# Optimization experiments

Hardware: AMD Instinct MI355X
Metric: run time of the kernel (lower is better)

## Reference

```python
import jax, jax.numpy as jnp
import numpy as np

NUM_HEADS = 8
HEAD_DIM = 96
SCALE = HEAD_DIM ** -0.5
STRIDE_Q = (1, 2, 2)
STRIDE_KV = (1, 8, 8)
PAD = [(1, 1), (1, 1), (1, 1)]  # kernel 3 -> padding = 3//2 = 1


def _gelu_pool(t, w, stride, thw):
    """_pre_attention_pool -> GELU -> depthwise Conv3d -> _post_attention_pool.

    t: [B, H, L, hd] flattened tokens; thw = (T, Hs, Ws) with L = T*Hs*Ws.
    Returns pooled [B, H, L', hd] and new thw.
    """
    B, NH, L, C = t.shape
    T, Hs, Ws = thw
    x = t.reshape(B * NH, T, Hs, Ws, C).transpose(0, 4, 1, 2, 3)  # [B*NH, C, T, Hs, Ws]
    x = jax.nn.gelu(x, approximate=False)  # torch F.gelu default (erf)
    x = jax.lax.conv_general_dilated(
        x, w, window_strides=stride, padding=PAD,
        dimension_numbers=('NCDHW', 'OIDHW', 'NCDHW'),
        feature_group_count=C)  # depthwise: groups = head_dim
    new_thw = (x.shape[2], x.shape[3], x.shape[4])
    Lp = new_thw[0] * new_thw[1] * new_thw[2]
    x = x.reshape(B, NH, C, Lp).transpose(0, 1, 3, 2)  # [B, NH, L', C]
    return x, new_thw


def setup_inputs() -> dict:
    key = jax.random.key(0)
    ks = jax.random.split(key, 8)
    B, T, Hs, Ws, C = 2, 8, 56, 56, 768
    L = T * Hs * Ws
    s = 0.02
    return {
        'x': jax.random.normal(ks[0], (B, L, C), jnp.float32),
        'qkv_w': jax.random.normal(ks[1], (3 * C, C), jnp.float32) * s,
        'qkv_b': jnp.zeros((3 * C,), jnp.float32),
        'proj_w': jax.random.normal(ks[2], (C, C), jnp.float32) * s,
        'proj_b': jnp.zeros((C,), jnp.float32),
        'pool_q_w': jax.random.normal(ks[3], (HEAD_DIM, 1, 3, 3, 3), jnp.float32) * 0.1,
        'pool_k_w': jax.random.normal(ks[4], (HEAD_DIM, 1, 3, 3, 3), jnp.float32) * 0.1,
        'pool_v_w': jax.random.normal(ks[5], (HEAD_DIM, 1, 3, 3, 3), jnp.float32) * 0.1,
        't_size': T, 'h_size': Hs, 'w_size': Ws,
    }


def reference(x, qkv_w, qkv_b, proj_w, proj_b, pool_q_w, pool_k_w, pool_v_w,
              t_size, h_size, w_size):
    B, N, C = x.shape
    # fused qkv projection -> [3, B, heads, N, head_dim]
    qkv = (x @ qkv_w.T + qkv_b).reshape(B, N, 3, NUM_HEADS, C // NUM_HEADS)
    qkv = qkv.transpose(2, 0, 3, 1, 4)
    q, k, v = qkv[0], qkv[1], qkv[2]

    thw = (t_size, h_size, w_size)
    q, q_thw = _gelu_pool(q, pool_q_w, STRIDE_Q, thw)
    k, _ = _gelu_pool(k, pool_k_w, STRIDE_KV, thw)
    v, _ = _gelu_pool(v, pool_v_w, STRIDE_KV, thw)

    attn = jax.nn.softmax((q * SCALE) @ jnp.swapaxes(k, -2, -1), axis=-1)
    Nq = q.shape[2]
    out = (attn @ v + q)  # residual_pool=True (iMViT)
    out = out.transpose(0, 2, 1, 3).reshape(B, Nq, C)
    out = out @ proj_w.T + proj_b
    return out
```

## Files before the change

### kernel.cpp

```cpp
#include <hip/hip_runtime.h>
#include <cstdint>

#define NH 8
#define HD 96
#define CDIM 768
#define BQ 2
#define T0 8
#define H0 56
#define W0 56
#define L0 (T0*H0*W0)
#define HP_Q 28
#define WP_Q 28
#define LQ (T0*HP_Q*WP_Q)
#define HP_K 7
#define WP_K 7
#define LK (T0*HP_K*WP_K)
#define LKP 416
#define SCALE 0.10206207261596577f
#define NYC 20
#define MKV 6400

typedef __bf16 bf16;
typedef bf16 bf16x4 __attribute__((ext_vector_type(4)));
typedef bf16 bf16x8 __attribute__((ext_vector_type(8)));
typedef float f32x4 __attribute__((ext_vector_type(4)));
typedef float f4 __attribute__((ext_vector_type(4)));

#define GPTR(x) ((const __attribute__((address_space(1))) void*)(x))
#define LPTR(x) ((__attribute__((address_space(3))) void*)(x))

__device__ __forceinline__ float fast_gelu(float x) {
    float z = __builtin_fabsf(x) * 0.7071067811865476f;
    float p = 1.f + z*(0.278393f + z*(0.230389f + z*(0.000972f + z*0.078108f)));
    p = p * p;
    p = p * p;
    float e = 1.f - __builtin_amdgcn_rcpf(p);
    float erfv = (x < 0.f) ? -e : e;
    return 0.5f * x * (1.f + erfv);
}

#define NX4 9633792
#define NW4 442368
#define NP4 147456
__global__ void cvt_all(const f4* __restrict__ x, const f4* __restrict__ wq,
                        const f4* __restrict__ wp, bf16x4* __restrict__ xo,
                        bf16x4* __restrict__ wqo, bf16x4* __restrict__ wpo) {
    const long total = (long)NX4 + NW4 + NP4;
    long stride = (long)gridDim.x * blockDim.x;
    for (long i = (long)blockIdx.x * blockDim.x + threadIdx.x; i < total; i += stride) {
        f4 v; bf16x4* o;
        if (i < NX4)            { v = x[i];            o = xo + i; }
        else if (i < NX4 + NW4) { v = wq[i - NX4];     o = wqo + (i - NX4); }
        else                    { v = wp[i - NX4 - NW4]; o = wpo + (i - NX4 - NW4); }
        bf16x4 t;
        t.x = (bf16)v.x; t.y = (bf16)v.y; t.z = (bf16)v.z; t.w = (bf16)v.w;
        *o = t;
    }
}

__device__ __forceinline__ int cmap(int i) {
    return ((i + 1) / 3) * 8 + (i + 1) % 3 - 1;
}

__global__ __launch_bounds__(512, 2) void gemm256_q(
    const bf16* __restrict__ A, const bf16* __restrict__ B,
    const float* __restrict__ bias, bf16* __restrict__ Out)
{
    __shared__ bf16 sh[2*32768];
    const int tid = threadIdx.x;
    const int lane = tid & 63;
    const int wid = tid >> 6;
    const int wm = wid >> 2, wn = wid & 3;
    const int arow = lane & 15;
    const int g = lane >> 4;
    const int srow = tid >> 3;
    const int schunk = tid & 7;
    const int csw = schunk ^ (srow & 7);
    const int K = 768;

    const int nwg = gridDim.x;
    const int q_ = nwg >> 3, r_ = nwg & 7;
    const int xcd = blockIdx.x & 7, off = blockIdx.x >> 3;
    const int swz = (xcd < r_ ? xcd*(q_+1) : r_*(q_+1) + (xcd - r_)*q_) + off;
    const long bn = swz % 3, bm = swz / 3;

    f32x4 acc[8][4];
#pragma unroll
    for (int i = 0; i < 8; ++i)
#pragma unroll
        for (int j = 0; j < 4; ++j) acc[i][j] = (f32x4){0.f,0.f,0.f,0.f};

    const bf16* Ab = A + (bm*256 + srow)*(long)K + csw*8;
    const bf16* Bb = B + (bn*256 + srow)*(long)K + csw*8;

    auto issueA = [&](int buf, int kt, int s) {
        __builtin_amdgcn_global_load_lds(GPTR(Ab + (long)(s*64)*K + kt*64),
            LPTR(sh + buf*32768 + s*4096 + tid*8), 16, 0, 0);
    };
    auto issueB = [&](int buf, int kt, int s) {
        __builtin_amdgcn_global_load_lds(GPTR(Bb + (long)(s*64)*K + kt*64),
            LPTR(sh + buf*32768 + 16384 + s*4096 + tid*8), 16, 0, 0);
    };
    auto phase = [&](int buf, int qm, int qn) {
        const bf16* ldsA = sh + buf*32768;
        const bf16* ldsB = sh + buf*32768 + 16384;
        bf16x8 af[4][2], bfr[2][2];
#pragma unroll
        for (int i = 0; i < 4; ++i) {
            int R = wm*128 + (qm*4 + i)*16 + arow;
#pragma unroll
            for (int kk = 0; kk < 2; ++kk)
                af[i][kk] = *(const bf16x8*)&ldsA[R*64 + (((kk*4 + g) ^ (R & 7))*8)];
        }
#pragma unroll
        for (int j = 0; j < 2; ++j) {
            int R = wn*64 + (qn*2 + j)*16 + arow;
#pragma unroll
            for (int kk = 0; kk < 2; ++kk)
                bfr[j][kk] = *(const bf16x8*)&ldsB[R*64 + (((kk*4 + g) ^ (R & 7))*8)];
        }
        asm volatile("s_waitcnt lgkmcnt(0)" ::: "memory");
        __builtin_amdgcn_sched_barrier(0);
        __builtin_amdgcn_s_setprio(1);
#pragma unroll
        for (int i = 0; i < 4; ++i)
#pragma unroll
            for (int j = 0; j < 2; ++j)
#pragma unroll
                for (int kk = 0; kk < 2; ++kk)
                    acc[qm*4 + i][qn*2 + j] = __builtin_amdgcn_mfma_f32_16x16x32_bf16(
                        af[i][kk], bfr[j][kk], acc[qm*4 + i][qn*2 + j], 0, 0, 0);
        __builtin_amdgcn_s_setprio(0);
        __builtin_amdgcn_sched_barrier(0);
    };

    const int nkt = K / 64;
#pragma unroll
    for (int s = 0; s < 4; ++s) { issueA(0, 0, s); issueB(0, 0, s); }

    for (int kt = 0; kt < nkt; ++kt) {
        const int cur = kt & 1, nxt = cur ^ 1;
        const bool pre = (kt + 1 < nkt);
        if (pre) { issueA(nxt, kt+1, 0); issueA(nxt, kt+1, 1); }
        if (pre) asm volatile("s_waitcnt vmcnt(2)" ::: "memory");
        else     asm volatile("s_waitcnt vmcnt(0)" ::: "memory");
        __builtin_amdgcn_s_barrier();
        phase(cur, 0, 0);
        if (pre) { issueA(nxt, kt+1, 2); issueA(nxt, kt+1, 3); }
        phase(cur, 0, 1);
        if (pre) { issueB(nxt, kt+1, 0); issueB(nxt, kt+1, 1); }
        phase(cur, 1, 0);
        if (pre) { issueB(nxt, kt+1, 2); issueB(nxt, kt+1, 3); }
        phase(cur, 1, 1);
        __builtin_amdgcn_s_barrier();
    }

    bf16* tls = sh;
#pragma unroll 1
    for (int half = 0; half < 2; ++half) {
        __syncthreads();
        if (wm == half) {
#pragma unroll
            for (int mf = 0; mf < 8; ++mf) {
                int rowl = mf*16 + (g << 2);
#pragma unroll
                for (int nf = 0; nf < 4; ++nf) {
                    int coll = wn*64 + nf*16 + arow;
                    float bcol = bias[bn*256 + coll];
#pragma unroll
                    for (int r = 0; r < 4; ++r)
                        tls[(rowl + r)*264 + coll] = (bf16)fast_gelu(acc[mf][nf][r] + bcol);
                }
            }
        }
        __syncthreads();
#pragma unroll
        for (int it = 0; it < 8; ++it) {
            int idx = it*512 + tid;
            int mloc = idx >> 5;
            int ck = idx & 31;
            bf16x8 v = *(const bf16x8*)&tls[mloc*264 + ck*8];
            int m = (int)bm*256 + half*128 + mloc;
            int col = (int)bn*256 + ck*8;
            int nh = col / HD;
            int c = col - nh*HD;
            int bflag = m >= L0;
            int l = m - (bflag ? L0 : 0);
            size_t addr = ((size_t)(bflag*8 + nh)*L0 + l)*HD + c;
            *(bf16x8*)&Out[addr] = v;
        }
    }
}

template<int MODE>
__global__ __launch_bounds__(256) void gemm_bt(
    const bf16* __restrict__ A, const bf16* __restrict__ B,
    const float* __restrict__ bias, void* __restrict__ Out,
    int M, int N, int K, int NBN)
{
    __shared__ bf16 sh[2*16384];
    const int tid = threadIdx.x;
    const int lane = tid & 63;
    const int w = tid >> 6;
    const int wr = w >> 1, wc = w & 1;

    const int nwg = gridDim.x;
    const int q_ = nwg >> 3, r_ = nwg & 7;
    const int xcd = blockIdx.x & 7, off = blockIdx.x >> 3;
    const int swz = (xcd < r_ ? xcd*(q_+1) : r_*(q_+1) + (xcd - r_)*q_) + off;
    const long bn = swz % NBN, bm = swz / NBN;

    f32x4 acc[4][4];
#pragma unroll
    for (int i = 0; i < 4; ++i)
#pragma unroll
        for (int j = 0; j < 4; ++j) acc[i][j] = (f32x4){0.f,0.f,0.f,0.f};

    const int trow = tid >> 3;
    const int tchunk = (tid & 7) ^ (trow & 7);

    long aoff[4];
#pragma unroll
    for (int s = 0; s < 4; ++s) {
        int rA = (int)bm*128 + s*32 + trow;
        if (MODE == 2) {
            int b = rA / 3200; int r = rA - b*3200;
            int t = r / 400;  int rr = r - t*400;
            int yi = rr / NYC, xi = rr - yi*NYC;
            int y = cmap(yi), x = cmap(xi);
            aoff[s] = ((long)b*L0 + (t*H0 + y)*W0 + x) * (long)K;
        } else {
            aoff[s] = (long)rA * K;
        }
    }
    const bf16* Bg = B + (bn*128 + trow)*(long)K + tchunk*8;

    const int arow = lane & 15;
    const int g8 = (lane >> 4) * 8;
    const int aswz = (arow & 7) * 8;

    auto stage = [&](int buf, int kt) {
        bf16* ldsA = sh + buf*16384;
        bf16* ldsB = sh + buf*16384 + 8192;
#pragma unroll
        for (int s = 0; s < 4; ++s) {
            __builtin_amdgcn_global_load_lds(GPTR(A + aoff[s] + kt*64 + tchunk*8),
                                             LPTR(ldsA + s*2048 + tid*8), 16, 0, 0);
            __builtin_amdgcn_global_load_lds(GPTR(Bg + (long)kt*64 + (long)s*32*K),
                                             LPTR(ldsB + s*2048 + tid*8), 16, 0, 0);
        }
    };
    auto compute = [&](int buf) {
        const bf16* ldsA = sh + buf*16384;
        const bf16* ldsB = sh + buf*16384 + 8192;
#pragma unroll
        for (int kk = 0; kk < 2; ++kk) {
            bf16x8 af[4], bfr[4];
#pragma unroll
            for (int i = 0; i < 4; ++i)
                af[i] = *(const bf16x8*)&ldsA[(wr*64 + i*16 + arow)*64 + ((kk*32 + g8) ^ aswz)];
#pragma unroll
            for (int j = 0; j < 4; ++j)
                bfr[j] = *(const bf16x8*)&ldsB[(wc*64 + j*16 + arow)*64 + ((kk*32 + g8) ^ aswz)];
            __builtin_amdgcn_s_setprio(1);
#pragma unroll
            for (int i = 0; i < 4; ++i)
#pragma unroll
                for (int j = 0; j < 4; ++j)
                    acc[i][j] = __builtin_amdgcn_mfma_f32_16x16x32_bf16(af[i], bfr[j], acc[i][j], 0, 0, 0);
            __builtin_amdgcn_s_setprio(0);
        }
    };

    const int nkt = K / 64;
    stage(0, 0);
    for (int kt = 0; kt < nkt; ++kt) {
        if (kt + 1 < nkt) {
            stage((kt + 1) & 1, kt + 1);
            asm volatile("s_waitcnt vmcnt(8)" ::: "memory");
        } else {
            asm volatile("s_waitcnt vmcnt(0)" ::: "memory");
        }
        __builtin_amdgcn_s_barrier();
        __builtin_amdgcn_sched_barrier(0);
        compute(kt & 1);
        __builtin_amdgcn_sched_barrier(0);
        __builtin_amdgcn_s_barrier();
    }

    if (MODE == 1) {
#pragma unroll
        for (int j = 0; j < 4; ++j) {
            const int col = (int)bn*128 + wc*64 + j*16 + (lane & 15);
            const float bcol = bias[col];
#pragma unroll
            for (int i = 0; i < 4; ++i) {
                int row0 = (int)bm*128 + wr*64 + i*16 + ((lane>>4)<<2);
#pragma unroll
                for (int r = 0; r < 4; ++r)
                    ((float*)Out)[(size_t)(row0 + r)*N + col] = acc[i][j][r] + bcol;
            }
        }
    } else {
        bf16* tls = sh;
#pragma unroll
        for (int j = 0; j < 4; ++j) {
            const int colb = (int)bn*128 + wc*64 + j*16;
            const int lcol = wc*64 + j*16 + (lane & 15);
            const float bcol = bias[colb + (lane & 15)];
#pragma unroll
            for (int i = 0; i < 4; ++i) {
                int lrow0 = wr*64 + i*16 + ((lane>>4)<<2);
#pragma unroll
                for (int r = 0; r < 4; ++r)
                    tls[(lrow0 + r)*136 + lcol] = (bf16)fast_gelu(acc[i][j][r] + bcol);
            }
        }
        __syncthreads();
#pragma unroll
        for (int it = 0; it < 8; ++it) {
            int idx = it*256 + tid;
            int mloc = idx >> 4;
            int ck = idx & 15;
            bf16x8 v = *(const bf16x8*)&tls[mloc*136 + ck*8];
            int m = (int)bm*128 + mloc;
            int col = (int)bn*128 + ck*8;
            int part = col / 768;
            int cb = col - part*768;
            int nh = cb / HD;
            int c = cb - nh*HD;
            int b = m / 3200; int r = m - b*3200;
            size_t addr = ((size_t)(part*16 + b*8 + nh)*3200 + r)*HD + c;
            *(bf16x8*)&((bf16*)Out)[addr] = v;
        }
    }
}

__global__ __launch_bounds__(256) void dwconv_q(
    const bf16* __restrict__ in, const float* __restrict__ w,
    bf16* __restrict__ out, int total)
{
    __shared__ float lw[27*HD];
    for (int i = threadIdx.x; i < 27*HD; i += 256) {
        int c = i / 27, tap = i % 27;
        lw[tap*HD + c] = w[i];
    }
    __syncthreads();
    int idx = blockIdx.x*256 + threadIdx.x;
    if (idx >= total) return;
    int c8 = idx % 12;
    int p = idx / 12;
    int xo = p % WP_Q;
    int yo = (p / WP_Q) % HP_Q;
    int bh = p / (WP_Q*HP_Q);
    const bf16* ip = in + (size_t)bh * L0 * HD + c8*8;

    float acc[T0][8];
#pragma unroll
    for (int t = 0; t < T0; ++t)
#pragma unroll
        for (int j = 0; j < 8; ++j) acc[t][j] = 0.f;

#pragma unroll
    for (int dy = 0; dy < 3; ++dy) {
        int y = yo*2 + dy - 1;
        if ((unsigned)y >= (unsigned)H0) continue;
#pragma unroll
        for (int dx = 0; dx < 3; ++dx) {
            int x = xo*2 + dx - 1;
            if ((unsigned)x >= (unsigned)W0) continue;
            float wreg[3][8];
#pragma unroll
            for (int dt = 0; dt < 3; ++dt)
#pragma unroll
                for (int j = 0; j < 8; ++j)
                    wreg[dt][j] = lw[(dt*9 + dy*3 + dx)*HD + c8*8 + j];
            const bf16* colp = ip + ((size_t)(y*W0 + x))*HD;
#pragma unroll
            for (int t = 0; t < T0; ++t) {
                bf16x8 v = *(const bf16x8*)(colp + (size_t)t*H0*W0*HD);
                float f[8];
#pragma unroll
                for (int j = 0; j < 8; ++j) f[j] = (float)v[j];
#pragma unroll
                for (int dt = 0; dt < 3; ++dt) {
                    int to = t - dt + 1;
                    if (to < 0 || to >= T0) continue;
#pragma unroll
                    for (int j = 0; j < 8; ++j)
                        acc[to][j] += wreg[dt][j] * f[j];
                }
            }
        }
    }

#pragma unroll
    for (int to = 0; to < T0; ++to) {
        int l = (to*HP_Q + yo)*WP_Q + xo;
        bf16x8 ov;
#pragma unroll
        for (int j = 0; j < 8; ++j) ov[j] = (bf16)acc[to][j];
        *(bf16x8*)&out[((size_t)bh*LQ + l)*HD + c8*8] = ov;
    }
}

__global__ __launch_bounds__(256) void dwconv_kv_all(
    const bf16* __restrict__ kv, const float* __restrict__ wk,
    const float* __restrict__ wv, bf16* __restrict__ kout, bf16* __restrict__ vtout)
{
    const int seg = blockIdx.x / 40;
    const int lb  = blockIdx.x % 40;
    const float* w = seg ? wv : wk;
    const bf16* in = kv + (size_t)seg * 16 * 3200 * HD;
    __shared__ float lw[27*HD];
    for (int i = threadIdx.x; i < 27*HD; i += 256) {
        int c = i / 27, tap = i % 27;
        lw[tap*HD + c] = w[i];
    }
    __syncthreads();

    if (lb >= 37) {
        int pid = (lb - 37)*256 + threadIdx.x;
        if (seg == 0) {
            for (int e = pid; e < 16*24*96; e += 768) {
                int bh = e / (24*96); int rem = e - bh*24*96;
                int l = LK + rem / 96; int c = rem % 96;
                kout[((size_t)bh*LKP + l)*HD + c] = (bf16)0.f;
            }
        } else {
            for (int e = pid; e < 16*96*24; e += 768) {
                int bh = e / (96*24); int rem = e - bh*96*24;
                int c = rem / 24; int l = LK + rem % 24;
                vtout[((size_t)bh*HD + c)*LKP + l] = (bf16)0.f;
            }
        }
        return;
    }

    int idx = lb*256 + threadIdx.x;
    if (idx >= 16*HP_K*WP_K*12) return;
    int c8 = idx % 12;
    int p = idx / 12;
    int xo = p % WP_K;
    int yo = (p / WP_K) % HP_K;
    int bh = p / (WP_K*HP_K);
    const bf16* ip = in + (size_t)bh * 3200 * HD + c8*8;

    float acc[T0][8];
#pragma unroll
    for (int t = 0; t < T0; ++t)
#pragma unroll
        for (int j = 0; j < 8; ++j) acc[t][j] = 0.f;

#pragma unroll
    for (int dy = 0; dy < 3; ++dy) {
        int yi = 3*yo + dy - 1;
        if ((unsigned)yi >= (unsigned)NYC) continue;
#pragma unroll
        for (int dx = 0; dx < 3; ++dx) {
            int xi = 3*xo + dx - 1;
            if ((unsigned)xi >= (unsigned)NYC) continue;
            float wreg[3][8];
#pragma unroll
            for (int dt = 0; dt < 3; ++dt)
#pragma unroll
                for (int j = 0; j < 8; ++j)
                    wreg[dt][j] = lw[(dt*9 + dy*3 + dx)*HD + c8*8 + j];
            const bf16* colp = ip + ((size_t)(yi*NYC + xi))*HD;
#pragma unroll
            for (int t = 0; t < T0; ++t) {
                bf16x8 v = *(const bf16x8*)(colp + (size_t)t*400*HD);
                float f[8];
#pragma unroll
                for (int j = 0; j < 8; ++j) f[j] = (float)v[j];
#pragma unroll
                for (int dt = 0; dt < 3; ++dt) {
                    int to = t - dt + 1;
                    if (to < 0 || to >= T0) continue;
#pragma unroll
                    for (int j = 0; j < 8; ++j)
                        acc[to][j] += wreg[dt][j] * f[j];
                }
            }
        }
    }

#pragma unroll
    for (int to = 0; to < T0; ++to) {
        int l = (to*HP_K + yo)*WP_K + xo;
        if (seg == 1) {
#pragma unroll
            for (int j = 0; j < 8; ++j)
                vtout[((size_t)bh*HD + c8*8 + j)*LKP + l] = (bf16)acc[to][j];
        } else {
            bf16x8 ov;
#pragma unroll
            for (int j = 0; j < 8; ++j) ov[j] = (bf16)acc[to][j];
            *(bf16x8*)&kout[((size_t)bh*LKP + l)*HD + c8*8] = ov;
        }
    }
}

__global__ __launch_bounds__(256) void attn_mfma(
    const bf16* __restrict__ q, const bf16* __restrict__ k,
    const bf16* __restrict__ vt, bf16* __restrict__ out)
{
    const int tid = threadIdx.x;
    const int lane = tid & 63;
    const int w = tid >> 6;
    const int col = lane & 15;
    const int g = lane >> 4;
    const int blk = blockIdx.x;
    const int qblk = blk % (LQ/64);
    const int bh = blk / (LQ/64);
    const int q0 = qblk*64 + w*16;

    const bf16* Qp  = q  + ((size_t)bh*LQ + q0)*HD;
    const bf16* Kp  = k  + (size_t)bh*LKP*HD;
    const bf16* VTp = vt + (size_t)bh*HD*LKP;

    bf16x8 qf[3];
#pragma unroll
    for (int c = 0; c < 3; ++c)
        qf[c] = *(const bf16x8*)&Qp[(size_t)col*HD + c*32 + g*8];

    f32x4 o[6];
#pragma unroll
    for (int t = 0; t < 6; ++t) o[t] = (f32x4){0.f,0.f,0.f,0.f};
    float lsum = 0.f;

    for (int kc = 0; kc < LKP/32; ++kc) {
        const int kvb = kc*32;
        uint32_t P[2][2];
#pragma unroll
        for (int s = 0; s < 2; ++s) {
            f32x4 acc = (f32x4){0.f,0.f,0.f,0.f};
#pragma unroll
            for (int c = 0; c < 3; ++c) {
                bf16x8 kf = *(const bf16x8*)&Kp[(size_t)(kvb + s*16 + col)*HD + c*32 + g*8];
                acc = __builtin_amdgcn_mfma_f32_16x16x32_bf16(kf, qf[c], acc, 0, 0, 0);
            }
            bf16x4 pb;
#pragma unroll
            for (int r = 0; r < 4; ++r) {
                int kv = kvb + s*16 + g*4 + r;
                float p = (kv < LK) ? __expf(acc[r]*SCALE) : 0.f;
                lsum += p;
                pb[r] = (bf16)p;
            }
            union { bf16x4 v; uint32_t u[2]; } pk; pk.v = pb;
            P[s][0] = pk.u[0]; P[s][1] = pk.u[1];
        }
        uint32_t sa0 = (g < 2) ? P[1][0] : P[0][0];
        uint32_t sa1 = (g < 2) ? P[1][1] : P[0][1];
        uint32_t tb0 = (g < 2) ? P[0][0] : P[1][0];
        uint32_t tb1 = (g < 2) ? P[0][1] : P[1][1];
        uint32_t R32_0 = (uint32_t)__shfl_xor((int)sa0, 32);
        uint32_t R32_1 = (uint32_t)__shfl_xor((int)sa1, 32);
        uint32_t R48_0 = (uint32_t)__shfl_xor((int)sa0, 48);
        uint32_t R48_1 = (uint32_t)__shfl_xor((int)sa1, 48);
        uint32_t R16_0 = (uint32_t)__shfl_xor((int)tb0, 16);
        uint32_t R16_1 = (uint32_t)__shfl_xor((int)tb1, 16);
        union { uint32_t u[4]; bf16x8 v; } pf;
        pf.u[0] = (g == 0) ? P[0][0] : (g == 1) ? R48_0 : (g == 2) ? R32_0 : R16_0;
        pf.u[1] = (g == 0) ? P[0][1] : (g == 1) ? R48_1 : (g == 2) ? R32_1 : R16_1;
        pf.u[2] = (g == 0) ? R16_0 : (g == 1) ? R32_0 : (g == 2) ? R48_0 : P[1][0];
        pf.u[3] = (g == 0) ? R16_1 : (g == 1) ? R32_1 : (g == 2) ? R48_1 : P[1][1];
#pragma unroll
        for (int t = 0; t < 6; ++t) {
            bf16x8 vf = *(const bf16x8*)&VTp[(size_t)(t*16 + col)*LKP + kvb + g*8];
            o[t] = __builtin_amdgcn_mfma_f32_16x16x32_bf16(vf, pf.v, o[t], 0, 0, 0);
        }
    }

    lsum += __shfl_xor(lsum, 16);
    lsum += __shfl_xor(lsum, 32);
    float inv = 1.f / lsum;

    const int b = bh >> 3, nh = bh & 7;
    size_t obase = ((size_t)b*LQ + q0 + col)*CDIM + (size_t)nh*HD;
#pragma unroll
    for (int t = 0; t < 6; ++t) {
        bf16x4 qres = *(const bf16x4*)&Qp[(size_t)col*HD + t*16 + g*4];
        bf16x4 ov;
#pragma unroll
        for (int r = 0; r < 4; ++r)
            ov[r] = (bf16)(o[t][r]*inv + (float)qres[r]);
        *(bf16x4*)&out[obase + t*16 + g*4] = ov;
    }
}

extern "C" void kernel_launch(void* const* d_in, const int* in_sizes, int n_in,
                              void* d_out, int out_size, void* d_ws, size_t ws_size,
                              hipStream_t stream) {
    const float* x      = (const float*)d_in[0];
    const float* qkv_w  = (const float*)d_in[1];
    const float* qkv_b  = (const float*)d_in[2];
    const float* proj_w = (const float*)d_in[3];
    const float* proj_b = (const float*)d_in[4];
    const float* pq_w   = (const float*)d_in[5];
    const float* pk_w   = (const float*)d_in[6];
    const float* pv_w   = (const float*)d_in[7];

    uint8_t* ws = (uint8_t*)d_ws;
    bf16* x_bf     = (bf16*)(ws);
    bf16* qg_out   = (bf16*)(ws +  77070336);
    bf16* kv_c     = (bf16*)(ws + 154140672);
    bf16* wqkv_bf  = (bf16*)(ws + 173801472);
    bf16* wproj_bf = (bf16*)(ws + 177340416);
    bf16* q_bf     = (bf16*)(ws + 178520064);
    bf16* k_bf     = (bf16*)(ws + 197787648);
    bf16* vt_bf    = (bf16*)(ws + 199065600);
    bf16* attn_o   = (bf16*)(ws + 200343552);

    cvt_all<<<2560, 256, 0, stream>>>((const f4*)x, (const f4*)qkv_w, (const f4*)proj_w,
                                      (bf16x4*)x_bf, (bf16x4*)wqkv_bf, (bf16x4*)wproj_bf);

    gemm256_q<<<196*3, 512, 0, stream>>>(x_bf, wqkv_bf, qkv_b, qg_out);

    gemm_bt<2><<<50*12, 256, 0, stream>>>(
        x_bf, wqkv_bf + (size_t)768*768, qkv_b + 768, kv_c, MKV, 1536, 768, 12);

    dwconv_q<<<588, 256, 0, stream>>>(qg_out, pq_w, q_bf, 16*HP_Q*WP_Q*12);
    dwconv_kv_all<<<80, 256, 0, stream>>>(kv_c, pk_w, pv_w, k_bf, vt_bf);

    attn_mfma<<<16*(LQ/64), 256, 0, stream>>>(q_bf, k_bf, vt_bf, attn_o);

    gemm_bt<1><<<6*98, 256, 0, stream>>>(
        attn_o, wproj_bf, proj_b, d_out, 12544, 768, 768, 6);
}
```

Baseline: 326.3 us.

## Fuse fp32-to-bf16 conversion of x into QKV GEMM A-tile loads

Removes the standalone pass that converted the whole 77MB fp32 input x to bf16. The Q and KV GEMMs now stream fp32 A tiles straight into LDS and convert them to bf16 while building MFMA fragments. The Q GEMM also drops its 256x256 tile for a 128x128 tile with K-step 32. This saves a full read and write of x, but doubles A-side LDS/global traffic per tile and adds conversion ALU work inside the inner loop.

```diff
diff --git a/kernel.cpp b/kernel.cpp
--- a/kernel.cpp
+++ b/kernel.cpp
@@ -39,21 +39,18 @@
     return 0.5f * x * (1.f + erfv);
 }
 
-#define NX4 9633792
 #define NW4 442368
 #define NP4 147456
-__global__ void cvt_all(const f4* __restrict__ x, const f4* __restrict__ wq,
-                        const f4* __restrict__ wp, bf16x4* __restrict__ xo,
-                        bf16x4* __restrict__ wqo, bf16x4* __restrict__ wpo) {
-    const long total = (long)NX4 + NW4 + NP4;
+__global__ void cvt_w(const f4* __restrict__ wq, const f4* __restrict__ wp,
+                      bf16x4* __restrict__ wqo, bf16x4* __restrict__ wpo) {
+    const long total = NW4 + NP4;
     long stride = (long)gridDim.x * blockDim.x;
     for (long i = (long)blockIdx.x * blockDim.x + threadIdx.x; i < total; i += stride) {
         f4 v; bf16x4* o;
-        if (i < NX4)            { v = x[i];            o = xo + i; }
-        else if (i < NX4 + NW4) { v = wq[i - NX4];     o = wqo + (i - NX4); }
-        else                    { v = wp[i - NX4 - NW4]; o = wpo + (i - NX4 - NW4); }
+        if (i < NW4) { v = wq[i]; o = wqo + i; }
+        else         { v = wp[i - NW4]; o = wpo + (i - NW4); }
         bf16x4 t;
-        t.x = (bf16)v.x; t.y = (bf16)v.y; t.z = (bf16)v.z; t.w = (bf16)v.w;
+        t[0] = (bf16)v[0]; t[1] = (bf16)v[1]; t[2] = (bf16)v[2]; t[3] = (bf16)v[3];
         *o = t;
     }
 }
@@ -62,140 +59,151 @@
     return ((i + 1) / 3) * 8 + (i + 1) % 3 - 1;
 }
 
-__global__ __launch_bounds__(512, 2) void gemm256_q(
-    const bf16* __restrict__ A, const bf16* __restrict__ B,
-    const float* __restrict__ bias, bf16* __restrict__ Out)
+template<int MODE>
+__global__ __launch_bounds__(256) void gemm_f32a(
+    const float* __restrict__ A, const bf16* __restrict__ B,
+    const float* __restrict__ bias, bf16* __restrict__ Out,
+    int M, int N, int K, int NBN)
 {
-    __shared__ bf16 sh[2*32768];
+    __shared__ uint8_t sh[2*24576];
     const int tid = threadIdx.x;
     const int lane = tid & 63;
-    const int wid = tid >> 6;
-    const int wm = wid >> 2, wn = wid & 3;
-    const int arow = lane & 15;
+    const int w = tid >> 6;
+    const int wr = w >> 1, wc = w & 1;
     const int g = lane >> 4;
-    const int srow = tid >> 3;
-    const int schunk = tid & 7;
-    const int csw = schunk ^ (srow & 7);
-    const int K = 768;
+    const int ar = lane & 15;
 
     const int nwg = gridDim.x;
     const int q_ = nwg >> 3, r_ = nwg & 7;
     const int xcd = blockIdx.x & 7, off = blockIdx.x >> 3;
     const int swz = (xcd < r_ ? xcd*(q_+1) : r_*(q_+1) + (xcd - r_)*q_) + off;
-    const long bn = swz % 3, bm = swz / 3;
-
-    f32x4 acc[8][4];
-#pragma unroll
-    for (int i = 0; i < 8; ++i)
+    const long bn = swz % NBN, bm = swz / NBN;
+
+    f32x4 acc[4][4];
+#pragma unroll
+    for (int i = 0; i < 4; ++i)
 #pragma unroll
         for (int j = 0; j < 4; ++j) acc[i][j] = (f32x4){0.f,0.f,0.f,0.f};
 
-    const bf16* Ab = A + (bm*256 + srow)*(long)K + csw*8;
-    const bf16* Bb = B + (bn*256 + srow)*(long)K + csw*8;
-
-    auto issueA = [&](int buf, int kt, int s) {
-        __builtin_amdgcn_global_load_lds(GPTR(Ab + (long)(s*64)*K + kt*64),
-            LPTR(sh + buf*32768 + s*4096 + tid*8), 16, 0, 0);
+    const int arow_s = tid >> 3;
+    const int csa = (tid & 7) ^ (arow_s & 7);
+    long aoff[4];
+#pragma unroll
+    for (int s = 0; s < 4; ++s) {
+        int rA = (int)bm*128 + s*32 + arow_s;
+        if (MODE == 2) {
+            int b = rA / 3200; int r = rA - b*3200;
+            int t = r / 400;  int rr = r - t*400;
+            int yi = rr / NYC, xi = rr - yi*NYC;
+            aoff[s] = ((long)b*L0 + (t*H0 + cmap(yi))*W0 + cmap(xi)) * (long)K;
+        } else {
+            aoff[s] = (long)rA * K;
+        }
+    }
+    const int brow_s = tid >> 2;
+    const int csb = (tid & 3) ^ ((tid >> 3) & 3);
+    const bf16* Bg = B + (bn*128 + brow_s)*(long)K + csb*8;
+
+    auto stage = [&](int buf, int kt) {
+        uint8_t* base = sh + buf*24576;
+#pragma unroll
+        for (int s = 0; s < 4; ++s)
+            __builtin_amdgcn_global_load_lds(GPTR(A + aoff[s] + kt*32 + csa*4),
+                LPTR(base + s*4096 + tid*16), 16, 0, 0);
+#pragma unroll
+        for (int s = 0; s < 2; ++s)
+            __builtin_amdgcn_global_load_lds(GPTR(Bg + (long)kt*32 + (long)s*64*K),
+                LPTR(base + 16384 + s*4096 + tid*16), 16, 0, 0);
     };
-    auto issueB = [&](int buf, int kt, int s) {
-        __builtin_amdgcn_global_load_lds(GPTR(Bb + (long)(s*64)*K + kt*64),
-            LPTR(sh + buf*32768 + 16384 + s*4096 + tid*8), 16, 0, 0);
+    auto compute = [&](int buf) {
+        const float* ldsA = (const float*)(sh + buf*24576);
+        const bf16* ldsB = (const bf16*)(sh + buf*24576 + 16384);
+        bf16x8 af[4], bfr[4];
+#pragma unroll
+        for (int i = 0; i < 4; ++i) {
+            int R = wr*64 + i*16 + ar;
+            f32x4 lo = *(const f32x4*)&ldsA[R*32 + (((2*g    ) ^ (R & 7))*4)];
+            f32x4 hi = *(const f32x4*)&ldsA[R*32 + (((2*g + 1) ^ (R & 7))*4)];
+            bf16x8 t;
+            t[0] = (bf16)lo[0]; t[1] = (bf16)lo[1]; t[2] = (bf16)lo[2]; t[3] = (bf16)lo[3];
+            t[4] = (bf16)hi[0]; t[5] = (bf16)hi[1]; t[6] = (bf16)hi[2]; t[7] = (bf16)hi[3];
+            af[i] = t;
+        }
+#pragma unroll
+        for (int j = 0; j < 4; ++j) {
+            int R = wc*64 + j*16 + ar;
+            bfr[j] = *(const bf16x8*)&ldsB[R*32 + ((g ^ ((R >> 1) & 3))*8)];
+        }
+        __builtin_amdgcn_s_setprio(1);
+#pragma unroll
+        for (int i = 0; i < 4; ++i)
+#pragma unroll
+            for (int j = 0; j < 4; ++j)
+                acc[i][j] = __builtin_amdgcn_mfma_f32_16x16x32_bf16(af[i], bfr[j], acc[i][j], 0, 0, 0);
+        __builtin_amdgcn_s_setprio(0);
     };
-    auto phase = [&](int buf, int qm, int qn) {
-        const bf16* ldsA = sh + buf*32768;
-        const bf16* ldsB = sh + buf*32768 + 16384;
-        bf16x8 af[4][2], bfr[2][2];
+
+    const int nkt = K / 32;
+    stage(0, 0);
+    for (int kt = 0; kt < nkt; ++kt) {
+        if (kt + 1 < nkt) {
+            stage((kt + 1) & 1, kt + 1);
+            asm volatile("s_waitcnt vmcnt(6)" ::: "memory");
+        } else {
+            asm volatile("s_waitcnt vmcnt(0)" ::: "memory");
+        }
+        __builtin_amdgcn_s_barrier();
+        __builtin_amdgcn_sched_barrier(0);
+        compute(kt & 1);
+        __builtin_amdgcn_sched_barrier(0);
+        __builtin_amdgcn_s_barrier();
+    }
+
+    bf16* tls = (bf16*)sh;
+#pragma unroll
+    for (int j = 0; j < 4; ++j) {
+        const int colb = (int)bn*128 + wc*64 + j*16;
+        const int lcol = wc*64 + j*16 + ar;
+        const float bcol = bias[colb + ar];
 #pragma unroll
         for (int i = 0; i < 4; ++i) {
-            int R = wm*128 + (qm*4 + i)*16 + arow;
-#pragma unroll
-            for (int kk = 0; kk < 2; ++kk)
-                af[i][kk] = *(const bf16x8*)&ldsA[R*64 + (((kk*4 + g) ^ (R & 7))*8)];
-        }
-#pragma unroll
-        for (int j = 0; j < 2; ++j) {
-            int R = wn*64 + (qn*2 + j)*16 + arow;
-#pragma unroll
-            for (int kk = 0; kk < 2; ++kk)
-                bfr[j][kk] = *(const bf16x8*)&ldsB[R*64 + (((kk*4 + g) ^ (R & 7))*8)];
-        }
-        asm volatile("s_waitcnt lgkmcnt(0)" ::: "memory");
-        __builtin_amdgcn_sched_barrier(0);
-        __builtin_amdgcn_s_setprio(1);
-#pragma unroll
-        for (int i = 0; i < 4; ++i)
-#pragma unroll
-            for (int j = 0; j < 2; ++j)
-#pragma unroll
-                for (int kk = 0; kk < 2; ++kk)
-                    acc[qm*4 + i][qn*2 + j] = __builtin_amdgcn_mfma_f32_16x16x32_bf16(
-                        af[i][kk], bfr[j][kk], acc[qm*4 + i][qn*2 + j], 0, 0, 0);
-        __builtin_amdgcn_s_setprio(0);
-        __builtin_amdgcn_sched_barrier(0);
-    };
-
-    const int nkt = K / 64;
-#pragma unroll
-    for (int s = 0; s < 4; ++s) { issueA(0, 0, s); issueB(0, 0, s); }
-
-    for (int kt = 0; kt < nkt; ++kt) {
-        const int cur = kt & 1, nxt = cur ^ 1;
-        const bool pre = (kt + 1 < nkt);
-        if (pre) { issueA(nxt, kt+1, 0); issueA(nxt, kt+1, 1); }
-        if (pre) asm volatile("s_waitcnt vmcnt(2)" ::: "memory");
-        else     asm volatile("s_waitcnt vmcnt(0)" ::: "memory");
-        __builtin_amdgcn_s_barrier();
-        phase(cur, 0, 0);
-        if (pre) { issueA(nxt, kt+1, 2); issueA(nxt, kt+1, 3); }
-        phase(cur, 0, 1);
-        if (pre) { issueB(nxt, kt+1, 0); issueB(nxt, kt+1, 1); }
-        phase(cur, 1, 0);
-        if (pre) { issueB(nxt, kt+1, 2); issueB(nxt, kt+1, 3); }
-        phase(cur, 1, 1);
-        __builtin_amdgcn_s_barrier();
-    }
-
-    bf16* tls = sh;
-#pragma unroll 1
-    for (int half = 0; half < 2; ++half) {
-        __syncthreads();
-        if (wm == half) {
-#pragma unroll
-            for (int mf = 0; mf < 8; ++mf) {
-                int rowl = mf*16 + (g << 2);
-#pragma unroll
-                for (int nf = 0; nf < 4; ++nf) {
-                    int coll = wn*64 + nf*16 + arow;
-                    float bcol = bias[bn*256 + coll];
-#pragma unroll
-                    for (int r = 0; r < 4; ++r)
-                        tls[(rowl + r)*264 + coll] = (bf16)fast_gelu(acc[mf][nf][r] + bcol);
-                }
-            }
-        }
-        __syncthreads();
-#pragma unroll
-        for (int it = 0; it < 8; ++it) {
-            int idx = it*512 + tid;
-            int mloc = idx >> 5;
-            int ck = idx & 31;
-            bf16x8 v = *(const bf16x8*)&tls[mloc*264 + ck*8];
-            int m = (int)bm*256 + half*128 + mloc;
-            int col = (int)bn*256 + ck*8;
+            int lrow0 = wr*64 + i*16 + (g << 2);
+#pragma unroll
+            for (int r = 0; r < 4; ++r)
+                tls[(lrow0 + r)*136 + lcol] = (bf16)fast_gelu(acc[i][j][r] + bcol);
+        }
+    }
+    __syncthreads();
+#pragma unroll
+    for (int it = 0; it < 8; ++it) {
+        int idx = it*256 + tid;
+        int mloc = idx >> 4;
+        int ck = idx & 15;
+        bf16x8 v = *(const bf16x8*)&tls[mloc*136 + ck*8];
+        int m = (int)bm*128 + mloc;
+        int col = (int)bn*128 + ck*8;
+        if (MODE == 0) {
             int nh = col / HD;
             int c = col - nh*HD;
             int bflag = m >= L0;
             int l = m - (bflag ? L0 : 0);
             size_t addr = ((size_t)(bflag*8 + nh)*L0 + l)*HD + c;
             *(bf16x8*)&Out[addr] = v;
-        }
-    }
-}
-
-template<int MODE>
-__global__ __launch_bounds__(256) void gemm_bt(
+        } else {
+            int part = col / 768;
+            int cb = col - part*768;
+            int nh = cb / HD;
+            int c = cb - nh*HD;
+            int b = m / 3200; int r = m - b*3200;
+            size_t addr = ((size_t)(part*16 + b*8 + nh)*3200 + r)*HD + c;
+            *(bf16x8*)&Out[addr] = v;
+        }
+    }
+}
+
+__global__ __launch_bounds__(256) void gemm_proj(
     const bf16* __restrict__ A, const bf16* __restrict__ B,
-    const float* __restrict__ bias, void* __restrict__ Out,
+    const float* __restrict__ bias, float* __restrict__ Out,
     int M, int N, int K, int NBN)
 {
     __shared__ bf16 sh[2*16384];
@@ -218,21 +226,7 @@
 
     const int trow = tid >> 3;
     const int tchunk = (tid & 7) ^ (trow & 7);
-
-    long aoff[4];
-#pragma unroll
-    for (int s = 0; s < 4; ++s) {
-        int rA = (int)bm*128 + s*32 + trow;
-        if (MODE == 2) {
-            int b = rA / 3200; int r = rA - b*3200;
-            int t = r / 400;  int rr = r - t*400;
-            int yi = rr / NYC, xi = rr - yi*NYC;
-            int y = cmap(yi), x = cmap(xi);
-            aoff[s] = ((long)b*L0 + (t*H0 + y)*W0 + x) * (long)K;
-        } else {
-            aoff[s] = (long)rA * K;
-        }
-    }
+    const bf16* Ag = A + (bm*128 + trow)*(long)K + tchunk*8;
     const bf16* Bg = B + (bn*128 + trow)*(long)K + tchunk*8;
 
     const int arow = lane & 15;
@@ -244,7 +238,7 @@
         bf16* ldsB = sh + buf*16384 + 8192;
 #pragma unroll
         for (int s = 0; s < 4; ++s) {
-            __builtin_amdgcn_global_load_lds(GPTR(A + aoff[s] + kt*64 + tchunk*8),
+            __builtin_amdgcn_global_load_lds(GPTR(Ag + (long)kt*64 + (long)s*32*K),
                                              LPTR(ldsA + s*2048 + tid*8), 16, 0, 0);
             __builtin_amdgcn_global_load_lds(GPTR(Bg + (long)kt*64 + (long)s*32*K),
                                              LPTR(ldsB + s*2048 + tid*8), 16, 0, 0);
@@ -288,50 +282,16 @@
         __builtin_amdgcn_s_barrier();
     }
 
-    if (MODE == 1) {
-#pragma unroll
-        for (int j = 0; j < 4; ++j) {
-            const int col = (int)bn*128 + wc*64 + j*16 + (lane & 15);
-            const float bcol = bias[col];
-#pragma unroll
-            for (int i = 0; i < 4; ++i) {
-                int row0 = (int)bm*128 + wr*64 + i*16 + ((lane>>4)<<2);
-#pragma unroll
-                for (int r = 0; r < 4; ++r)
-                    ((float*)Out)[(size_t)(row0 + r)*N + col] = acc[i][j][r] + bcol;
-            }
-        }
-    } else {
-        bf16* tls = sh;
-#pragma unroll
-        for (int j = 0; j < 4; ++j) {
-            const int colb = (int)bn*128 + wc*64 + j*16;
-            const int lcol = wc*64 + j*16 + (lane & 15);
-            const float bcol = bias[colb + (lane & 15)];
-#pragma unroll
-            for (int i = 0; i < 4; ++i) {
-                int lrow0 = wr*64 + i*16 + ((lane>>4)<<2);
-#pragma unroll
-                for (int r = 0; r < 4; ++r)
-                    tls[(lrow0 + r)*136 + lcol] = (bf16)fast_gelu(acc[i][j][r] + bcol);
-            }
-        }
-        __syncthreads();
-#pragma unroll
-        for (int it = 0; it < 8; ++it) {
-            int idx = it*256 + tid;
-            int mloc = idx >> 4;
-            int ck = idx & 15;
-            bf16x8 v = *(const bf16x8*)&tls[mloc*136 + ck*8];
-            int m = (int)bm*128 + mloc;
-            int col = (int)bn*128 + ck*8;
-            int part = col / 768;
-            int cb = col - part*768;
-            int nh = cb / HD;
-            int c = cb - nh*HD;
-            int b = m / 3200; int r = m - b*3200;
-            size_t addr = ((size_t)(part*16 + b*8 + nh)*3200 + r)*HD + c;
-            *(bf16x8*)&((bf16*)Out)[addr] = v;
+#pragma unroll
+    for (int j = 0; j < 4; ++j) {
+        const int col = (int)bn*128 + wc*64 + j*16 + (lane & 15);
+        const float bcol = bias[col];
+#pragma unroll
+        for (int i = 0; i < 4; ++i) {
+            int row0 = (int)bm*128 + wr*64 + i*16 + ((lane>>4)<<2);
+#pragma unroll
+            for (int r = 0; r < 4; ++r)
+                Out[(size_t)(row0 + r)*N + col] = acc[i][j][r] + bcol;
         }
     }
 }
@@ -603,29 +563,29 @@
     const float* pv_w   = (const float*)d_in[7];
 
     uint8_t* ws = (uint8_t*)d_ws;
-    bf16* x_bf     = (bf16*)(ws);
-    bf16* qg_out   = (bf16*)(ws +  77070336);
-    bf16* kv_c     = (bf16*)(ws + 154140672);
-    bf16* wqkv_bf  = (bf16*)(ws + 173801472);
-    bf16* wproj_bf = (bf16*)(ws + 177340416);
-    bf16* q_bf     = (bf16*)(ws + 178520064);
-    bf16* k_bf     = (bf16*)(ws + 197787648);
-    bf16* vt_bf    = (bf16*)(ws + 199065600);
-    bf16* attn_o   = (bf16*)(ws + 200343552);
-
-    cvt_all<<<2560, 256, 0, stream>>>((const f4*)x, (const f4*)qkv_w, (const f4*)proj_w,
-                                      (bf16x4*)x_bf, (bf16x4*)wqkv_bf, (bf16x4*)wproj_bf);
-
-    gemm256_q<<<196*3, 512, 0, stream>>>(x_bf, wqkv_bf, qkv_b, qg_out);
-
-    gemm_bt<2><<<50*12, 256, 0, stream>>>(
-        x_bf, wqkv_bf + (size_t)768*768, qkv_b + 768, kv_c, MKV, 1536, 768, 12);
+    bf16* qg_out   = (bf16*)(ws);
+    bf16* kv_c     = (bf16*)(ws +  77070336);
+    bf16* wqkv_bf  = (bf16*)(ws +  96731136);
+    bf16* wproj_bf = (bf16*)(ws + 100270080);
+    bf16* q_bf     = (bf16*)(ws + 101449728);
+    bf16* k_bf     = (bf16*)(ws + 120717312);
+    bf16* vt_bf    = (bf16*)(ws + 121995264);
+    bf16* attn_o   = (bf16*)(ws + 123273216);
+
+    cvt_w<<<576, 256, 0, stream>>>((const f4*)qkv_w, (const f4*)proj_w,
+                                   (bf16x4*)wqkv_bf, (bf16x4*)wproj_bf);
+
+    gemm_f32a<0><<<392*6, 256, 0, stream>>>(
+        x, wqkv_bf, qkv_b, qg_out, 50176, 768, 768, 6);
+
+    gemm_f32a<2><<<50*12, 256, 0, stream>>>(
+        x, wqkv_bf + (size_t)768*768, qkv_b + 768, kv_c, MKV, 1536, 768, 12);
 
     dwconv_q<<<588, 256, 0, stream>>>(qg_out, pq_w, q_bf, 16*HP_Q*WP_Q*12);
     dwconv_kv_all<<<80, 256, 0, stream>>>(kv_c, pk_w, pv_w, k_bf, vt_bf);
 
     attn_mfma<<<16*(LQ/64), 256, 0, stream>>>(q_bf, k_bf, vt_bf, attn_o);
 
-    gemm_bt<1><<<6*98, 256, 0, stream>>>(
-        attn_o, wproj_bf, proj_b, d_out, 12544, 768, 768, 6);
-}
+    gemm_proj<<<6*98, 256, 0, stream>>>(
+        attn_o, wproj_bf, proj_b, (float*)d_out, 12544, 768, 768, 6);
+}
```

New measurement: 314.6 us. 3.6% less time.
